# Kernel optimization log

Measured on AMD Instinct MI355X. Metric: run time of the kernel, lower is better.

The kernel has to match this reference:

```python
import jax, jax.numpy as jnp
import numpy as np

DIM = 180
HEADS = 6
HEAD_DIM = DIM // HEADS
SCALE = HEAD_DIM ** (-0.5)
BW, N, K = 8192, 64, 16


def setup_inputs() -> dict:
    key = jax.random.key(0)
    ks = jax.random.split(key, 6)
    return {
        "x": jax.random.normal(ks[0], (BW, N, DIM), dtype=jnp.float32),
        "bpe_windows": jax.random.normal(ks[1], (BW, N, K), dtype=jnp.float32),
        "qkv_w": jax.random.normal(ks[2], (3 * DIM, DIM), dtype=jnp.float32) * 0.05,
        "qkv_b": jax.random.normal(ks[3], (3 * DIM,), dtype=jnp.float32) * 0.05,
        "proj_w": jax.random.normal(ks[4], (DIM, DIM), dtype=jnp.float32) * 0.05,
        "proj_b": jax.random.normal(ks[5], (DIM,), dtype=jnp.float32) * 0.05,
        "tau": jnp.ones((HEADS, 1, 1), dtype=jnp.float32),
    }


def reference(x, bpe_windows, qkv_w, qkv_b, proj_w, proj_b, tau):
    B_, n, C = x.shape
    # qkv projection -> (3, B_, H, N, hd)
    qkv = (x @ qkv_w.T + qkv_b).reshape(B_, n, 3, HEADS, HEAD_DIM)
    qkv = jnp.transpose(qkv, (2, 0, 3, 1, 4))
    q, k, v = qkv[0], qkv[1], qkv[2]
    q = q * SCALE
    attn = jnp.einsum("bhid,bhjd->bhij", q, k)  # (B_, H, N, N)
    # geodesic bias from BPE embeddings: d_B(i,j) = ||bpe_i - bpe_j||_2
    diff = bpe_windows[:, :, None, :] - bpe_windows[:, None, :, :]  # (B_, N, N, K)
    d_B = jnp.sqrt(jnp.sum(diff * diff, axis=-1))  # (B_, N, N)
    log_W_geo = -d_B[:, None, :, :] / jnp.clip(tau, 1e-6)[None]  # (B_, H, N, N)
    attn = jax.nn.softmax(attn + log_W_geo, axis=-1)
    out = jnp.einsum("bhij,bhjd->bhid", attn, v)  # (B_, H, N, hd)
    out = jnp.transpose(out, (0, 2, 1, 3)).reshape(B_, n, C)
    return out @ proj_w.T + proj_b
```

## Files before the change

kernel.cpp:

```cpp
#include <hip/hip_runtime.h>
#include <hip/hip_bf16.h>
#include <math.h>

typedef __attribute__((ext_vector_type(8))) short short8b;
typedef __attribute__((ext_vector_type(4))) float f32x4;
typedef __attribute__((ext_vector_type(4))) unsigned short ushort4b;
typedef __attribute__((ext_vector_type(2))) unsigned short ushort2b;

#define NWIN 8192
#define NT   512
#define SCALE 0.18257418583505536f

#define XB_P 200
#define QK_P 200
#define VT_P 72
#define BPE_P 36
#define ATT_P 184

#define OFF_XB  0
#define OFF_QK  25600
#define OFF_VT  51200
#define OFF_BPE 65024
#define OFF_N   69632
#define LDS_BYTES 69888

#define WK 192

__device__ __forceinline__ unsigned int bf2pk(float lo, float hi) {
    union { __hip_bfloat162 h; unsigned int u; } cv;
    cv.h = __float22bfloat162_rn(make_float2(lo, hi));
    return cv.u;
}
__device__ __forceinline__ unsigned short bf1(float v) {
    union { __hip_bfloat16 h; unsigned short u; } cv;
    cv.h = __float2bfloat16(v);
    return cv.u;
}

__global__ void prep_weights(const float* __restrict__ qkv_w,
                             const float* __restrict__ proj_w,
                             unsigned short* __restrict__ wqr,
                             unsigned short* __restrict__ wpr)
{
    const int idx = blockIdx.x * 256 + threadIdx.x;
    if (idx < 540 * WK) {
        const int r = idx / WK, k = idx % WK;
        const int seg = r / 30, dd = r % 30;
        const int which = seg / 6, hh = seg % 6;
        float v = 0.f;
        if (k < 180)
            v = qkv_w[(which * 180 + hh * 30 + dd) * 180 + k];
        wqr[idx] = bf1(v);
    }
    const int j = idx - 540 * WK;
    if (j >= 0 && j < WK * WK) {
        const int r = j / WK, k = j % WK;
        float v = 0.f;
        if (r < 180 && k < 180)
            v = proj_w[r * 180 + k];
        wpr[j] = bf1(v);
    }
}

__global__ void __launch_bounds__(NT, 4)
waga_mfma(const float* __restrict__ x,
          const float* __restrict__ bpe,
          const unsigned short* __restrict__ wqr,
          const unsigned short* __restrict__ wpr,
          const float* __restrict__ qkv_b,
          const float* __restrict__ proj_b,
          const float* __restrict__ tau,
          float* __restrict__ out)
{
    extern __shared__ char smem[];
    unsigned short* xb   = (unsigned short*)(smem + OFF_XB);
    unsigned short* qk   = (unsigned short*)(smem + OFF_QK);
    unsigned short* vT   = (unsigned short*)(smem + OFF_VT);
    unsigned short* bpeB = (unsigned short*)(smem + OFF_BPE);
    float*          nv   = (float*)(smem + OFF_N);

    const int b = blockIdx.x;
    const int t = threadIdx.x;
    const int w = t >> 6;
    const int l = t & 63;
    const int lr = l & 15;
    const int g  = l >> 4;

    unsigned short* attg = (unsigned short*)((char*)out + (size_t)b * 46080 + 22528);

    if (t < 192) {
        const int n = t / 3, c = t % 3;
        *reinterpret_cast<uint2*>(xb + n * XB_P + 180 + 4 * c) = make_uint2(0u, 0u);
    } else if (t < 256) {
        const int n = t - 192;
        ushort4b z = {0, 0, 0, 0};
        *reinterpret_cast<ushort4b*>(attg + n * ATT_P + 180) = z;
    } else if (t < 512) {
        const int i = t - 256;
        const int n = i >> 2, c4 = i & 3;
        ushort4b z = {0, 0, 0, 0};
        *reinterpret_cast<ushort4b*>(bpeB + n * BPE_P + 16 + 4 * c4) = z;
    }
    {
        const float* xw = x + (size_t)b * 11520;
        for (int i = t; i < 64 * 45; i += NT) {
            const int n = i / 45, c4 = i % 45;
            const float4 v = *reinterpret_cast<const float4*>(xw + i * 4);
            *reinterpret_cast<uint2*>(xb + n * XB_P + c4 * 4) =
                make_uint2(bf2pk(v.x, v.y), bf2pk(v.z, v.w));
        }
    }
    if (t < 256) {
        const float4 v = *reinterpret_cast<const float4*>(bpe + (size_t)b * 1024 + t * 4);
        *reinterpret_cast<uint2*>(bpeB + (t >> 2) * BPE_P + (t & 3) * 4) =
            make_uint2(bf2pk(v.x, v.y), bf2pk(v.z, v.w));
    }
    if (t < 64) {
        const float* bp = bpe + (size_t)b * 1024 + t * 16;
        float s = 0.f;
        #pragma unroll
        for (int k4 = 0; k4 < 4; ++k4) {
            const float4 v = *reinterpret_cast<const float4*>(bp + 4 * k4);
            s += v.x * v.x + v.y * v.y + v.z * v.z + v.w * v.w;
        }
        nv[t] = s;
    }
    __syncthreads();

    for (int pass = 0; pass < 2; ++pass) {
        if (pass) __syncthreads();

        {
            f32x4 acc[3][4];
            const unsigned short* wrow[3];
            bool has[3], arow_ok[3];
            int whichv[3], hhl[3], halfv[3];
            #pragma unroll
            for (int ti = 0; ti < 3; ++ti) {
                const int tl = w + 8 * ti;
                has[ti] = (tl < 18);
                const int tls = has[ti] ? tl : 0;
                const int segl = tls >> 1;
                halfv[ti] = tls & 1;
                whichv[ti] = segl / 3;
                hhl[ti] = segl % 3;
                const int hg = 3 * pass + hhl[ti];
                const int wseg = whichv[ti] * 6 + hg;
                const int ddr = halfv[ti] * 16 + lr;
                arow_ok[ti] = (ddr < 30);
                wrow[ti] = wqr + (size_t)(wseg * 30 + (arow_ok[ti] ? ddr : 0)) * WK;
                const int ddb = halfv[ti] * 16 + g * 4;
                const int cbase = whichv[ti] * 180 + hg * 30;
                f32x4 binit;
                #pragma unroll
                for (int i = 0; i < 4; ++i)
                    binit[i] = (ddb + i < 30) ? qkv_b[cbase + ddb + i] : 0.f;
                #pragma unroll
                for (int mt = 0; mt < 4; ++mt) acc[ti][mt] = binit;
            }
            #pragma unroll
            for (int kk = 0; kk < 6; ++kk) {
                short8b xf[4];
                #pragma unroll
                for (int mt = 0; mt < 4; ++mt)
                    xf[mt] = *reinterpret_cast<const short8b*>(
                        xb + (mt * 16 + lr) * XB_P + kk * 32 + g * 8);
                #pragma unroll
                for (int ti = 0; ti < 3; ++ti) {
                    if (!has[ti]) continue;
                    short8b wfv;
                    if (arow_ok[ti])
                        wfv = *reinterpret_cast<const short8b*>(wrow[ti] + kk * 32 + g * 8);
                    else
                        wfv = short8b{0, 0, 0, 0, 0, 0, 0, 0};
                    #pragma unroll
                    for (int mt = 0; mt < 4; ++mt)
                        acc[ti][mt] = __builtin_amdgcn_mfma_f32_16x16x32_bf16(
                            wfv, xf[mt], acc[ti][mt], 0, 0, 0);
                }
            }
            #pragma unroll
            for (int ti = 0; ti < 3; ++ti) {
                if (!has[ti]) continue;
                const int ddb = halfv[ti] * 16 + g * 4;
                #pragma unroll
                for (int mt = 0; mt < 4; ++mt) {
                    const int tok = mt * 16 + lr;
                    float v0 = acc[ti][mt][0], v1 = acc[ti][mt][1];
                    float v2 = acc[ti][mt][2], v3 = acc[ti][mt][3];
                    if (whichv[ti] == 0) { v0 *= SCALE; v1 *= SCALE; v2 *= SCALE; v3 *= SCALE; }
                    if (whichv[ti] < 2) {
                        *reinterpret_cast<uint2*>(
                            qk + tok * QK_P + hhl[ti] * 64 + whichv[ti] * 32 + ddb) =
                            make_uint2(bf2pk(v0, v1), bf2pk(v2, v3));
                    } else {
                        const int c = (tok & 32) + ((tok >> 2) & 3) * 8 + ((tok >> 4) & 1) * 4 + (tok & 3);
                        unsigned short* vb = vT + hhl[ti] * 2304 + ddb * VT_P + c;
                        vb[0 * VT_P] = bf1(v0);
                        vb[1 * VT_P] = bf1(v1);
                        vb[2 * VT_P] = bf1(v2);
                        vb[3 * VT_P] = bf1(v3);
                    }
                }
            }
        }
        __syncthreads();

        for (int u = w; u < 12; u += 8) {
            const int hh = u >> 2, mt = u & 3;
            const int h = 3 * pass + hh;
            const int tok = mt * 16 + lr;
            const unsigned short* qkh = qk + hh * 64;
            const short8b qf = *reinterpret_cast<const short8b*>(
                qkh + tok * QK_P + g * 8);
            short8b kf[4];
            #pragma unroll
            for (int jt = 0; jt < 4; ++jt)
                kf[jt] = *reinterpret_cast<const short8b*>(
                    qkh + (jt * 16 + lr) * QK_P + 32 + g * 8);
            short8b vf[2][2];
            #pragma unroll
            for (int ntd = 0; ntd < 2; ++ntd)
                #pragma unroll
                for (int ks = 0; ks < 2; ++ks)
                    vf[ntd][ks] = *reinterpret_cast<const short8b*>(
                        vT + hh * 2304 + (ntd * 16 + lr) * VT_P + ks * 32 + g * 8);
            const short8b btf = *reinterpret_cast<const short8b*>(
                bpeB + tok * BPE_P + g * 8);
            const f32x4 zero4 = {0.f, 0.f, 0.f, 0.f};
            f32x4 g2[4];
            #pragma unroll
            for (int jt = 0; jt < 4; ++jt) {
                const short8b baf = *reinterpret_cast<const short8b*>(
                    bpeB + (jt * 16 + lr) * BPE_P + g * 8);
                g2[jt] = __builtin_amdgcn_mfma_f32_16x16x32_bf16(baf, btf, zero4, 0, 0, 0);
            }
            const float itau = 1.f / fmaxf(tau[h], 1e-6f);
            const float ntok = nv[tok];
            f32x4 s[4];
            #pragma unroll
            for (int jt = 0; jt < 4; ++jt) {
                const f32x4 nj = *reinterpret_cast<const f32x4*>(nv + jt * 16 + g * 4);
                #pragma unroll
                for (int i = 0; i < 4; ++i) {
                    const int j = jt * 16 + g * 4 + i;
                    float d2 = fmaf(-2.f, g2[jt][i], ntok + nj[i]);
                    d2 = (j == tok) ? 0.f : fmaxf(d2, 0.f);
                    s[jt][i] = -itau * __builtin_sqrtf(d2);
                }
            }
            #pragma unroll
            for (int jt = 0; jt < 4; ++jt)
                s[jt] = __builtin_amdgcn_mfma_f32_16x16x32_bf16(kf[jt], qf, s[jt], 0, 0, 0);
            float m4[4], a4[4];
            #pragma unroll
            for (int i = 0; i < 4; ++i)
                m4[i] = fmaxf(fmaxf(s[0][i], s[1][i]), fmaxf(s[2][i], s[3][i]));
            float mx = fmaxf(fmaxf(m4[0], m4[1]), fmaxf(m4[2], m4[3]));
            mx = fmaxf(mx, __shfl_xor(mx, 16));
            mx = fmaxf(mx, __shfl_xor(mx, 32));
            #pragma unroll
            for (int jt = 0; jt < 4; ++jt)
                #pragma unroll
                for (int i = 0; i < 4; ++i)
                    s[jt][i] = __expf(s[jt][i] - mx);
            #pragma unroll
            for (int i = 0; i < 4; ++i)
                a4[i] = (s[0][i] + s[1][i]) + (s[2][i] + s[3][i]);
            float sum = (a4[0] + a4[1]) + (a4[2] + a4[3]);
            sum += __shfl_xor(sum, 16);
            sum += __shfl_xor(sum, 32);
            const float inv = 1.f / sum;
            union { short8b v; unsigned int u[4]; } pb[2];
            #pragma unroll
            for (int ks = 0; ks < 2; ++ks) {
                pb[ks].u[0] = bf2pk(s[2 * ks][0] * inv, s[2 * ks][1] * inv);
                pb[ks].u[1] = bf2pk(s[2 * ks][2] * inv, s[2 * ks][3] * inv);
                pb[ks].u[2] = bf2pk(s[2 * ks + 1][0] * inv, s[2 * ks + 1][1] * inv);
                pb[ks].u[3] = bf2pk(s[2 * ks + 1][2] * inv, s[2 * ks + 1][3] * inv);
            }
            #pragma unroll
            for (int ntd = 0; ntd < 2; ++ntd) {
                f32x4 o = {0.f, 0.f, 0.f, 0.f};
                o = __builtin_amdgcn_mfma_f32_16x16x32_bf16(vf[ntd][0], pb[0].v, o, 0, 0, 0);
                o = __builtin_amdgcn_mfma_f32_16x16x32_bf16(vf[ntd][1], pb[1].v, o, 0, 0, 0);
                const int col = h * 30 + ntd * 16 + g * 4;
                unsigned short* dst = attg + tok * ATT_P + col;
                if (ntd == 0 || g < 3) {
                    *reinterpret_cast<uint2*>(dst) =
                        make_uint2(bf2pk(o[0], o[1]), bf2pk(o[2], o[3]));
                } else {
                    *reinterpret_cast<unsigned int*>(dst) = bf2pk(o[0], o[1]);
                }
            }
        }
    }
    __syncthreads();

    {
        const int mt = w & 3;
        const int ntb = (w >> 2) * 6;
        short8b attf[6];
        #pragma unroll
        for (int kk = 0; kk < 6; ++kk) {
            if (kk == 5 && g == 3)
                attf[kk] = short8b{0, 0, 0, 0, 0, 0, 0, 0};
            else
                attf[kk] = *reinterpret_cast<const short8b*>(
                    attg + (mt * 16 + lr) * ATT_P + kk * 32 + g * 8);
        }
        f32x4 pacc[6];
        #pragma unroll
        for (int q6 = 0; q6 < 6; ++q6) {
            const int nt = ntb + q6;
            const unsigned short* wrow = wpr + (size_t)(nt * 16 + lr) * WK;
            const int cb = nt * 16 + g * 4;
            f32x4 acc;
            #pragma unroll
            for (int i = 0; i < 4; ++i)
                acc[i] = (cb + i < 180) ? proj_b[cb + i] : 0.f;
            #pragma unroll
            for (int kk = 0; kk < 6; ++kk) {
                const short8b wf = *reinterpret_cast<const short8b*>(wrow + kk * 32 + g * 8);
                acc = __builtin_amdgcn_mfma_f32_16x16x32_bf16(wf, attf[kk], acc, 0, 0, 0);
            }
            pacc[q6] = acc;
        }
        __syncthreads();
        #pragma unroll
        for (int q6 = 0; q6 < 6; ++q6) {
            const int nt = ntb + q6;
            const int cb = nt * 16 + g * 4;
            if (cb < 177) {
                const int tok = mt * 16 + lr;
                *reinterpret_cast<float4*>(out + ((size_t)b * 64 + tok) * 180 + cb) =
                    make_float4(pacc[q6][0], pacc[q6][1], pacc[q6][2], pacc[q6][3]);
            }
        }
    }
}

extern "C" void kernel_launch(void* const* d_in, const int* in_sizes, int n_in,
                              void* d_out, int out_size, void* d_ws, size_t ws_size,
                              hipStream_t stream) {
    (void)in_sizes; (void)n_in; (void)out_size; (void)ws_size;
    const float* x      = (const float*)d_in[0];
    const float* bpe    = (const float*)d_in[1];
    const float* qkv_w  = (const float*)d_in[2];
    const float* qkv_b  = (const float*)d_in[3];
    const float* proj_w = (const float*)d_in[4];
    const float* proj_b = (const float*)d_in[5];
    const float* tau    = (const float*)d_in[6];

    unsigned short* wqr = (unsigned short*)d_ws;
    unsigned short* wpr = wqr + 540 * WK;

    prep_weights<<<(540 * WK + WK * WK + 255) / 256, 256, 0, stream>>>(
        qkv_w, proj_w, wqr, wpr);

    (void)hipFuncSetAttribute((const void*)waga_mfma,
                              hipFuncAttributeMaxDynamicSharedMemorySize,
                              LDS_BYTES);
    waga_mfma<<<NWIN, NT, LDS_BYTES, stream>>>(x, bpe, wqr, wpr, qkv_b, proj_b, tau,
                                               (float*)d_out);
}
```

Baseline: 834.3 us.

## Precompute exact fp32 geodesic distances once per window into fp16 LDS table

```diff
diff --git a/kernel.cpp b/kernel.cpp
--- a/kernel.cpp
+++ b/kernel.cpp
@@ -1,11 +1,11 @@
 #include <hip/hip_runtime.h>
+#include <hip/hip_fp16.h>
 #include <hip/hip_bf16.h>
 #include <math.h>
 
 typedef __attribute__((ext_vector_type(8))) short short8b;
 typedef __attribute__((ext_vector_type(4))) float f32x4;
 typedef __attribute__((ext_vector_type(4))) unsigned short ushort4b;
-typedef __attribute__((ext_vector_type(2))) unsigned short ushort2b;
 
 #define NWIN 8192
 #define NT   512
@@ -14,15 +14,15 @@
 #define XB_P 200
 #define QK_P 200
 #define VT_P 72
-#define BPE_P 36
+#define DB_P 68
 #define ATT_P 184
 
 #define OFF_XB  0
 #define OFF_QK  25600
 #define OFF_VT  51200
-#define OFF_BPE 65024
-#define OFF_N   69632
-#define LDS_BYTES 69888
+#define OFF_DB  65024
+#define OFF_BPE 73728
+#define LDS_BYTES 78848
 
 #define WK 192
 
@@ -62,7 +62,7 @@
     }
 }
 
-__global__ void __launch_bounds__(NT, 4)
+__global__ void __launch_bounds__(NT, 3)
 waga_mfma(const float* __restrict__ x,
           const float* __restrict__ bpe,
           const unsigned short* __restrict__ wqr,
@@ -76,8 +76,8 @@
     unsigned short* xb   = (unsigned short*)(smem + OFF_XB);
     unsigned short* qk   = (unsigned short*)(smem + OFF_QK);
     unsigned short* vT   = (unsigned short*)(smem + OFF_VT);
-    unsigned short* bpeB = (unsigned short*)(smem + OFF_BPE);
-    float*          nv   = (float*)(smem + OFF_N);
+    unsigned short* dBs  = (unsigned short*)(smem + OFF_DB);
+    float*          bpes = (float*)(smem + OFF_BPE);
 
     const int b = blockIdx.x;
     const int t = threadIdx.x;
@@ -95,11 +95,6 @@
         const int n = t - 192;
         ushort4b z = {0, 0, 0, 0};
         *reinterpret_cast<ushort4b*>(attg + n * ATT_P + 180) = z;
-    } else if (t < 512) {
-        const int i = t - 256;
-        const int n = i >> 2, c4 = i & 3;
-        ushort4b z = {0, 0, 0, 0};
-        *reinterpret_cast<ushort4b*>(bpeB + n * BPE_P + 16 + 4 * c4) = z;
     }
     {
         const float* xw = x + (size_t)b * 11520;
@@ -112,20 +107,40 @@
     }
     if (t < 256) {
         const float4 v = *reinterpret_cast<const float4*>(bpe + (size_t)b * 1024 + t * 4);
-        *reinterpret_cast<uint2*>(bpeB + (t >> 2) * BPE_P + (t & 3) * 4) =
-            make_uint2(bf2pk(v.x, v.y), bf2pk(v.z, v.w));
-    }
-    if (t < 64) {
-        const float* bp = bpe + (size_t)b * 1024 + t * 16;
-        float s = 0.f;
+        *reinterpret_cast<float4*>(bpes + (t >> 2) * 20 + (t & 3) * 4) = v;
+    }
+    __syncthreads();
+
+    {
+        const int ti = t >> 4, tj = t & 15;
+        float acc0[4] = {0.f, 0.f, 0.f, 0.f};
+        float acc1[4] = {0.f, 0.f, 0.f, 0.f};
         #pragma unroll
         for (int k4 = 0; k4 < 4; ++k4) {
-            const float4 v = *reinterpret_cast<const float4*>(bp + 4 * k4);
-            s += v.x * v.x + v.y * v.y + v.z * v.z + v.w * v.w;
-        }
-        nv[t] = s;
-    }
-    __syncthreads();
+            const float4 a0 = *reinterpret_cast<const float4*>(bpes + ti * 20 + 4 * k4);
+            const float4 a1 = *reinterpret_cast<const float4*>(bpes + (ti + 32) * 20 + 4 * k4);
+            #pragma unroll
+            for (int e = 0; e < 4; ++e) {
+                const float4 bb = *reinterpret_cast<const float4*>(bpes + (tj + 16 * e) * 20 + 4 * k4);
+                float d;
+                d = a0.x - bb.x; acc0[e] += d * d;
+                d = a0.y - bb.y; acc0[e] += d * d;
+                d = a0.z - bb.z; acc0[e] += d * d;
+                d = a0.w - bb.w; acc0[e] += d * d;
+                d = a1.x - bb.x; acc1[e] += d * d;
+                d = a1.y - bb.y; acc1[e] += d * d;
+                d = a1.z - bb.z; acc1[e] += d * d;
+                d = a1.w - bb.w; acc1[e] += d * d;
+            }
+        }
+        #pragma unroll
+        for (int e = 0; e < 4; ++e) {
+            dBs[ti * DB_P + tj + 16 * e] =
+                __half_as_ushort(__float2half_rn(sqrtf(acc0[e])));
+            dBs[(ti + 32) * DB_P + tj + 16 * e] =
+                __half_as_ushort(__float2half_rn(sqrtf(acc1[e])));
+        }
+    }
 
     for (int pass = 0; pass < 2; ++pass) {
         if (pass) __syncthreads();
@@ -225,33 +240,21 @@
                 for (int ks = 0; ks < 2; ++ks)
                     vf[ntd][ks] = *reinterpret_cast<const short8b*>(
                         vT + hh * 2304 + (ntd * 16 + lr) * VT_P + ks * 32 + g * 8);
-            const short8b btf = *reinterpret_cast<const short8b*>(
-                bpeB + tok * BPE_P + g * 8);
-            const f32x4 zero4 = {0.f, 0.f, 0.f, 0.f};
-            f32x4 g2[4];
+            const float itau = 1.f / fmaxf(tau[h], 1e-6f);
+            f32x4 s[4];
             #pragma unroll
             for (int jt = 0; jt < 4; ++jt) {
-                const short8b baf = *reinterpret_cast<const short8b*>(
-                    bpeB + (jt * 16 + lr) * BPE_P + g * 8);
-                g2[jt] = __builtin_amdgcn_mfma_f32_16x16x32_bf16(baf, btf, zero4, 0, 0, 0);
-            }
-            const float itau = 1.f / fmaxf(tau[h], 1e-6f);
-            const float ntok = nv[tok];
-            f32x4 s[4];
-            #pragma unroll
-            for (int jt = 0; jt < 4; ++jt) {
-                const f32x4 nj = *reinterpret_cast<const f32x4*>(nv + jt * 16 + g * 4);
-                #pragma unroll
-                for (int i = 0; i < 4; ++i) {
-                    const int j = jt * 16 + g * 4 + i;
-                    float d2 = fmaf(-2.f, g2[jt][i], ntok + nj[i]);
-                    d2 = (j == tok) ? 0.f : fmaxf(d2, 0.f);
-                    s[jt][i] = -itau * __builtin_sqrtf(d2);
-                }
-            }
+                const ushort4b du = *reinterpret_cast<const ushort4b*>(
+                    dBs + tok * DB_P + jt * 16 + g * 4);
+                #pragma unroll
+                for (int i = 0; i < 4; ++i)
+                    s[jt][i] = -itau * __half2float(__ushort_as_half(du[i]));
+            }
+            __builtin_amdgcn_s_setprio(1);
             #pragma unroll
             for (int jt = 0; jt < 4; ++jt)
                 s[jt] = __builtin_amdgcn_mfma_f32_16x16x32_bf16(kf[jt], qf, s[jt], 0, 0, 0);
+            __builtin_amdgcn_s_setprio(0);
             float m4[4], a4[4];
             #pragma unroll
             for (int i = 0; i < 4; ++i)
@@ -279,18 +282,24 @@
                 pb[ks].u[2] = bf2pk(s[2 * ks + 1][0] * inv, s[2 * ks + 1][1] * inv);
                 pb[ks].u[3] = bf2pk(s[2 * ks + 1][2] * inv, s[2 * ks + 1][3] * inv);
             }
-            #pragma unroll
-            for (int ntd = 0; ntd < 2; ++ntd) {
-                f32x4 o = {0.f, 0.f, 0.f, 0.f};
-                o = __builtin_amdgcn_mfma_f32_16x16x32_bf16(vf[ntd][0], pb[0].v, o, 0, 0, 0);
-                o = __builtin_amdgcn_mfma_f32_16x16x32_bf16(vf[ntd][1], pb[1].v, o, 0, 0, 0);
-                const int col = h * 30 + ntd * 16 + g * 4;
-                unsigned short* dst = attg + tok * ATT_P + col;
-                if (ntd == 0 || g < 3) {
-                    *reinterpret_cast<uint2*>(dst) =
-                        make_uint2(bf2pk(o[0], o[1]), bf2pk(o[2], o[3]));
+            __builtin_amdgcn_s_setprio(1);
+            f32x4 o0 = {0.f, 0.f, 0.f, 0.f}, o1 = {0.f, 0.f, 0.f, 0.f};
+            o0 = __builtin_amdgcn_mfma_f32_16x16x32_bf16(vf[0][0], pb[0].v, o0, 0, 0, 0);
+            o1 = __builtin_amdgcn_mfma_f32_16x16x32_bf16(vf[1][0], pb[0].v, o1, 0, 0, 0);
+            o0 = __builtin_amdgcn_mfma_f32_16x16x32_bf16(vf[0][1], pb[1].v, o0, 0, 0, 0);
+            o1 = __builtin_amdgcn_mfma_f32_16x16x32_bf16(vf[1][1], pb[1].v, o1, 0, 0, 0);
+            __builtin_amdgcn_s_setprio(0);
+            {
+                const int col0 = h * 30 + g * 4;
+                *reinterpret_cast<uint2*>(attg + tok * ATT_P + col0) =
+                    make_uint2(bf2pk(o0[0], o0[1]), bf2pk(o0[2], o0[3]));
+                const int col1 = h * 30 + 16 + g * 4;
+                if (g < 3) {
+                    *reinterpret_cast<uint2*>(attg + tok * ATT_P + col1) =
+                        make_uint2(bf2pk(o1[0], o1[1]), bf2pk(o1[2], o1[3]));
                 } else {
-                    *reinterpret_cast<unsigned int*>(dst) = bf2pk(o[0], o[1]);
+                    *reinterpret_cast<unsigned int*>(attg + tok * ATT_P + col1) =
+                        bf2pk(o1[0], o1[1]);
                 }
             }
         }
@@ -310,27 +319,37 @@
                     attg + (mt * 16 + lr) * ATT_P + kk * 32 + g * 8);
         }
         f32x4 pacc[6];
+        short8b wf[6];
+        #pragma unroll
+        for (int kk = 0; kk < 6; ++kk)
+            wf[kk] = *reinterpret_cast<const short8b*>(
+                wpr + (size_t)(ntb * 16 + lr) * WK + kk * 32 + g * 8);
         #pragma unroll
         for (int q6 = 0; q6 < 6; ++q6) {
-            const int nt = ntb + q6;
-            const unsigned short* wrow = wpr + (size_t)(nt * 16 + lr) * WK;
-            const int cb = nt * 16 + g * 4;
+            short8b wcur[6];
+            #pragma unroll
+            for (int kk = 0; kk < 6; ++kk) wcur[kk] = wf[kk];
+            if (q6 < 5) {
+                const unsigned short* wrown =
+                    wpr + (size_t)((ntb + q6 + 1) * 16 + lr) * WK;
+                #pragma unroll
+                for (int kk = 0; kk < 6; ++kk)
+                    wf[kk] = *reinterpret_cast<const short8b*>(wrown + kk * 32 + g * 8);
+            }
+            const int cb = (ntb + q6) * 16 + g * 4;
             f32x4 acc;
             #pragma unroll
             for (int i = 0; i < 4; ++i)
                 acc[i] = (cb + i < 180) ? proj_b[cb + i] : 0.f;
             #pragma unroll
-            for (int kk = 0; kk < 6; ++kk) {
-                const short8b wf = *reinterpret_cast<const short8b*>(wrow + kk * 32 + g * 8);
-                acc = __builtin_amdgcn_mfma_f32_16x16x32_bf16(wf, attf[kk], acc, 0, 0, 0);
-            }
+            for (int kk = 0; kk < 6; ++kk)
+                acc = __builtin_amdgcn_mfma_f32_16x16x32_bf16(wcur[kk], attf[kk], acc, 0, 0, 0);
             pacc[q6] = acc;
         }
         __syncthreads();
         #pragma unroll
         for (int q6 = 0; q6 < 6; ++q6) {
-            const int nt = ntb + q6;
-            const int cb = nt * 16 + g * 4;
+            const int cb = (ntb + q6) * 16 + g * 4;
             if (cb < 177) {
                 const int tok = mt * 16 + lr;
                 *reinterpret_cast<float4*>(out + ((size_t)b * 64 + tok) * 180 + cb) =
```

After: 737.0 us. 11.7% less time.
